# Kernel tuning notes

Hardware: AMD Instinct MI355X
Metric: run time of the kernel (lower is better)

The kernel has to match this reference:

```python
import jax, jax.numpy as jnp
import numpy as np

NUM_HEADS = 16


def setup_inputs() -> dict:
    key = jax.random.key(0)
    ks = jax.random.split(key, 5)
    B, S, E = 4, 2048, 1024
    scale = 1.0 / np.sqrt(E)
    return {
        "query": jax.random.normal(ks[0], (B, S, E), dtype=jnp.float32),
        "w_in": jax.random.normal(ks[1], (3 * E, E), dtype=jnp.float32) * scale,
        "b_in": jax.random.normal(ks[2], (3 * E,), dtype=jnp.float32) * 0.02,
        "w_out": jax.random.normal(ks[3], (E, E), dtype=jnp.float32) * scale,
        "b_out": jax.random.normal(ks[4], (E,), dtype=jnp.float32) * 0.02,
    }


def reference(query, w_in, b_in, w_out, b_out):
    B, S, E = query.shape
    H = NUM_HEADS
    D = E // H
    # fused QKV projection: [B,S,3E]
    qkv = jnp.einsum('bse,fe->bsf', query, w_in) + b_in
    q, k, v = jnp.split(qkv, 3, axis=-1)
    # [B,H,S,D]
    q = q.reshape(B, S, H, D).transpose(0, 2, 1, 3)
    k = k.reshape(B, S, H, D).transpose(0, 2, 1, 3)
    v = v.reshape(B, S, H, D).transpose(0, 2, 1, 3)
    # scaled dot-product attention with causal mask (is_causal=True, dropout=0)
    scores = jnp.einsum('bhqd,bhkd->bhqk', q, k) * (1.0 / np.sqrt(D))
    causal = jnp.tril(jnp.ones((S, S), dtype=bool))
    scores = jnp.where(causal, scores, jnp.finfo(scores.dtype).min)
    probs = jax.nn.softmax(scores, axis=-1)
    attn = jnp.einsum('bhqk,bhkd->bhqd', probs, v)
    attn = attn.transpose(0, 2, 1, 3).reshape(B, S, E)
    return jnp.einsum('bse,fe->bsf', attn, w_out) + b_out
```

## Files before the change

### kernel.cpp

```cpp
#include <hip/hip_runtime.h>

typedef __bf16 bf16;
typedef __bf16 bf16x4 __attribute__((ext_vector_type(4)));
typedef __bf16 bf16x8 __attribute__((ext_vector_type(8)));
typedef float  f32x4  __attribute__((ext_vector_type(4)));
typedef short  short4v __attribute__((ext_vector_type(4)));

#define GLOAD_LDS16(g, l) __builtin_amdgcn_global_load_lds( \
    (const __attribute__((address_space(1))) void*)(g),     \
    (__attribute__((address_space(3))) void*)(l), 16, 0, 0)

__device__ __forceinline__ float exp2_hw(float x) { return __builtin_amdgcn_exp2f(x); }

#if __has_builtin(__builtin_amdgcn_mfma_f32_16x16x16bf16_1k)
__device__ __forceinline__ f32x4 mfma16(bf16x4 a, bf16x4 b, f32x4 c) {
    return __builtin_amdgcn_mfma_f32_16x16x16bf16_1k(
        __builtin_bit_cast(short4v, a), __builtin_bit_cast(short4v, b), c, 0, 0, 0);
}
#elif __has_builtin(__builtin_amdgcn_mfma_f32_16x16x16_bf16)
__device__ __forceinline__ f32x4 mfma16(bf16x4 a, bf16x4 b, f32x4 c) {
    return __builtin_amdgcn_mfma_f32_16x16x16_bf16(a, b, c, 0, 0, 0);
}
#else
__device__ __forceinline__ f32x4 mfma16(bf16x4 a, bf16x4 b, f32x4 c) {
    asm volatile("v_mfma_f32_16x16x16_bf16 %0, %1, %2, %0"
                 : "+v"(c) : "v"(a), "v"(b));
    return c;
}
#endif

__global__ __launch_bounds__(256) void f32_to_bf16(
    const float* __restrict__ in, bf16* __restrict__ out, int n4)
{
    int i = blockIdx.x * blockDim.x + threadIdx.x;
    const int stride = gridDim.x * blockDim.x;
    for (; i < n4; i += stride) {
        const float4 v = *(const float4*)(in + (size_t)i * 4);
        bf16x4 o = { (bf16)v.x, (bf16)v.y, (bf16)v.z, (bf16)v.w };
        *(bf16x4*)(out + (size_t)i * 4) = o;
    }
}

__global__ __launch_bounds__(256) void conv_rest(
    const float* __restrict__ w_in_f, const float* __restrict__ b_in_f,
    const float* __restrict__ w_out_f, const float* __restrict__ b_out_f,
    bf16* __restrict__ w_in, bf16* __restrict__ b_in,
    bf16* __restrict__ w_out, bf16* __restrict__ b_out)
{
    constexpr int N1 = 786432, N2 = N1 + 768, N3 = N2 + 262144, N4 = N3 + 256;
    int i = blockIdx.x * blockDim.x + threadIdx.x;
    const int stride = gridDim.x * blockDim.x;
    for (; i < N4; i += stride) {
        const float* src; bf16* dst; int off;
        if (i < N1)      { src = w_in_f;  dst = w_in;  off = i; }
        else if (i < N2) { src = b_in_f;  dst = b_in;  off = i - N1; }
        else if (i < N3) { src = w_out_f; dst = w_out; off = i - N2; }
        else             { src = b_out_f; dst = b_out; off = i - N3; }
        const float4 v = *(const float4*)(src + (size_t)off * 4);
        bf16x4 o = { (bf16)v.x, (bf16)v.y, (bf16)v.z, (bf16)v.w };
        *(bf16x4*)(dst + (size_t)off * 4) = o;
    }
}

__device__ __forceinline__ void gemm_mainloop_128(
    const bf16* __restrict__ A, const bf16* __restrict__ B, int K,
    int bm, int bn, bf16* As, bf16* Bs, f32x4 (&acc)[4][4])
{
    const int tid  = threadIdx.x;
    const int lane = tid & 63, fr = lane & 15, fq = lane >> 4;
    const int wave = tid >> 6;
    const int wr   = (wave >> 1) * 64, wc = (wave & 1) * 64;
    const int srow = tid >> 3, sj = tid & 7;
    const int sjs  = (sj ^ (srow & 7)) * 8;
    const int xo0  = (fq ^ (fr & 7)) * 8;
    const int xo1  = ((4 + fq) ^ (fr & 7)) * 8;

    const bf16* Ag = A + (size_t)(bm * 128 + srow) * K + sjs;
    const bf16* Bg = B + (size_t)(bn * 128 + srow) * K + sjs;
    bf16* Asw = As + srow * 64 + sj * 8;
    bf16* Bsw = Bs + srow * 64 + sj * 8;

    for (int k0 = 0; k0 < K; k0 += 64) {
        __syncthreads();
#pragma unroll
        for (int it = 0; it < 4; ++it)
            GLOAD_LDS16(Ag + k0 + (size_t)it * 32 * K, Asw + it * 32 * 64);
#pragma unroll
        for (int it = 0; it < 4; ++it)
            GLOAD_LDS16(Bg + k0 + (size_t)it * 32 * K, Bsw + it * 32 * 64);
        asm volatile("s_waitcnt vmcnt(0)" ::: "memory");
        __syncthreads();

#pragma unroll
        for (int ks = 0; ks < 2; ++ks) {
            const int xo = ks ? xo1 : xo0;
            bf16x8 a[4], b[4];
#pragma unroll
            for (int m = 0; m < 4; ++m)
                a[m] = *(const bf16x8*)&As[(wr + m * 16 + fr) * 64 + xo];
#pragma unroll
            for (int n = 0; n < 4; ++n)
                b[n] = *(const bf16x8*)&Bs[(wc + n * 16 + fr) * 64 + xo];
#pragma unroll
            for (int m = 0; m < 4; ++m)
#pragma unroll
                for (int n = 0; n < 4; ++n)
                    acc[m][n] = __builtin_amdgcn_mfma_f32_16x16x32_bf16(a[m], b[n], acc[m][n], 0, 0, 0);
        }
    }
}

__global__ __launch_bounds__(256) void gemm_qkv(
    const bf16* __restrict__ A, const bf16* __restrict__ B,
    const bf16* __restrict__ bias,
    bf16* __restrict__ qb_, bf16* __restrict__ kb_, bf16* __restrict__ vt_)
{
    constexpr int K = 1024, NTN = 24;
    constexpr float QSCALE = 0.18033688011112042f;
    __shared__ bf16 As[128 * 64];
    __shared__ bf16 Bs[128 * 64];
    const int bm = blockIdx.x / NTN, bn = blockIdx.x % NTN;

    f32x4 acc[4][4] = {};
    gemm_mainloop_128(A, B, K, bm, bn, As, Bs, acc);

    const int tid = threadIdx.x, lane = tid & 63;
    const int fr = lane & 15, fq = lane >> 4;
    const int wave = tid >> 6;
    const int wr = (wave >> 1) * 64, wc = (wave & 1) * 64;

    const int colbase = bn * 128 + wc;
    const int part = colbase >> 10;

#pragma unroll
    for (int n = 0; n < 4; ++n) {
        const int col = colbase + n * 16 + fr;
        const float bv = (float)bias[col];
        const int cl = col & 1023, h = cl >> 6, d = cl & 63;
#pragma unroll
        for (int m = 0; m < 4; ++m) {
            const int row0 = bm * 128 + wr + m * 16 + fq * 4;
            const int bb = row0 >> 11, s0 = row0 & 2047;
            const int bh = bb * 16 + h;
            if (part == 0) {
#pragma unroll
                for (int j = 0; j < 4; ++j)
                    qb_[((size_t)bh * 2048 + s0 + j) * 64 + d] = (bf16)((acc[m][n][j] + bv) * QSCALE);
            } else if (part == 1) {
#pragma unroll
                for (int j = 0; j < 4; ++j)
                    kb_[((size_t)bh * 2048 + s0 + j) * 64 + d] = (bf16)(acc[m][n][j] + bv);
            } else {
                bf16x4 o;
#pragma unroll
                for (int j = 0; j < 4; ++j) o[j] = (bf16)(acc[m][n][j] + bv);
                *(bf16x4*)&vt_[((size_t)bh * 64 + d) * 2048 + s0] = o;
            }
        }
    }
}

__global__ __launch_bounds__(256) void gemm_out(
    const bf16* __restrict__ A, const bf16* __restrict__ B,
    const bf16* __restrict__ bias, float* __restrict__ C)
{
    constexpr int K = 1024, N = 1024, NTN = 8;
    __shared__ bf16 As[128 * 64];
    __shared__ bf16 Bs[128 * 64];
    const int bm = blockIdx.x / NTN, bn = blockIdx.x % NTN;

    f32x4 acc[4][4] = {};
    gemm_mainloop_128(A, B, K, bm, bn, As, Bs, acc);

    const int tid = threadIdx.x, lane = tid & 63;
    const int fr = lane & 15, fq = lane >> 4;
    const int wave = tid >> 6;
    const int wr = (wave >> 1) * 64, wc = (wave & 1) * 64;

#pragma unroll
    for (int n = 0; n < 4; ++n) {
        const int col = bn * 128 + wc + n * 16 + fr;
        const float bv = (float)bias[col];
#pragma unroll
        for (int m = 0; m < 4; ++m) {
            const int row0 = bm * 128 + wr + m * 16 + fq * 4;
#pragma unroll
            for (int j = 0; j < 4; ++j)
                C[(size_t)(row0 + j) * N + col] = acc[m][n][j] + bv;
        }
    }
}

__global__ __launch_bounds__(256) void attn4(
    const bf16* __restrict__ qb_, const bf16* __restrict__ kb_,
    const bf16* __restrict__ vt_, bf16* __restrict__ ctx)
{
    constexpr int S = 2048, EO = 1024;
    constexpr float NEG = -3.0e38f;
    __shared__ bf16 Ks[2][64 * 64];
    __shared__ bf16 Vs[2][64 * 64];

    const int idx = blockIdx.x;
    const int orig = (idx & 7) * 256 + (idx >> 3);
    const int bh = orig >> 5;
    const int qb = 31 - (orig & 31);
    const int bb = bh >> 4, h = bh & 15;

    const int tid = threadIdx.x, lane = tid & 63, wave = tid >> 6;
    const int fr = lane & 15, fq = lane >> 4;

    const bf16* kh = kb_ + (size_t)bh * S * 64;
    const bf16* vh = vt_ + (size_t)bh * 64 * S;
    const bf16* qh = qb_ + (size_t)bh * S * 64;

    const int q0 = qb * 64 + wave * 16;

    bf16x8 qf0, qf1;
    {
        const bf16* qr = qh + (size_t)(q0 + fr) * 64;
        qf0 = *(const bf16x8*)(qr + fq * 8);
        qf1 = *(const bf16x8*)(qr + 32 + fq * 8);
    }

    const int xo0 = (fq ^ (fr & 7)) * 8;
    const int xo1 = ((4 + fq) ^ (fr & 7)) * 8;

    int krb[4], vslot[4], vrow[4];
#pragma unroll
    for (int n = 0; n < 4; ++n) {
        krb[n]   = (n * 16 + fr) * 64;
        vslot[n] = ((n * 2 + (fq >> 1)) ^ (fr & 7)) * 8 + (fq & 1) * 4;
        vrow[n]  = (n * 16 + fr) * 64;
    }

    const int r0 = tid >> 3, j0 = tid & 7;
    const int js = (j0 ^ (r0 & 7)) * 8;

#define STAGE(buf, kt)                                                              \
    do {                                                                            \
        GLOAD_LDS16(kh + (size_t)((kt) * 64 + r0) * 64 + js, &Ks[buf][(r0 * 8 + j0) * 8]);        \
        GLOAD_LDS16(kh + (size_t)((kt) * 64 + r0 + 32) * 64 + js, &Ks[buf][((r0 + 32) * 8 + j0) * 8]); \
        GLOAD_LDS16(vh + (size_t)r0 * S + (kt) * 64 + js, &Vs[buf][(r0 * 8 + j0) * 8]);           \
        GLOAD_LDS16(vh + (size_t)(r0 + 32) * S + (kt) * 64 + js, &Vs[buf][((r0 + 32) * 8 + j0) * 8]); \
    } while (0)

    f32x4 acc[4] = {};
    float lrow = 0.0f;

    STAGE(0, 0);
    asm volatile("s_waitcnt vmcnt(0)" ::: "memory");
    __syncthreads();

    int cur = 0;
    for (int kt = 0; kt <= qb; ++kt) {
        if (kt < qb) STAGE(cur ^ 1, kt + 1);

        f32x4 s[4] = {};
        __builtin_amdgcn_s_setprio(1);
#pragma unroll
        for (int n = 0; n < 4; ++n) {
            bf16x8 k0v = *(const bf16x8*)&Ks[cur][krb[n] + xo0];
            bf16x8 k1v = *(const bf16x8*)&Ks[cur][krb[n] + xo1];
            s[n] = __builtin_amdgcn_mfma_f32_16x16x32_bf16(k0v, qf0, s[n], 0, 0, 0);
            s[n] = __builtin_amdgcn_mfma_f32_16x16x32_bf16(k1v, qf1, s[n], 0, 0, 0);
        }
        __builtin_amdgcn_s_setprio(0);

        if (kt == qb) {
            const int qrel = wave * 16 + fr;
#pragma unroll
            for (int n = 0; n < 4; ++n)
#pragma unroll
                for (int j = 0; j < 4; ++j)
                    if (n * 16 + fq * 4 + j > qrel) s[n][j] = NEG;
        }

        bf16x4 pb[4];
        float rs = 0.0f;
#pragma unroll
        for (int n = 0; n < 4; ++n) {
            float p0 = exp2_hw(s[n][0]);
            float p1 = exp2_hw(s[n][1]);
            float p2 = exp2_hw(s[n][2]);
            float p3 = exp2_hw(s[n][3]);
            pb[n][0] = (bf16)p0; pb[n][1] = (bf16)p1;
            pb[n][2] = (bf16)p2; pb[n][3] = (bf16)p3;
            rs += (p0 + p1) + (p2 + p3);
        }
        lrow += rs;

        __builtin_amdgcn_s_setprio(1);
#pragma unroll
        for (int n = 0; n < 4; ++n) {
#pragma unroll
            for (int n2 = 0; n2 < 4; ++n2) {
                bf16x4 vf = *(const bf16x4*)&Vs[cur][vrow[n2] + vslot[n]];
                acc[n2] = mfma16(pb[n], vf, acc[n2]);
            }
        }
        __builtin_amdgcn_s_setprio(0);

        asm volatile("s_waitcnt vmcnt(0)" ::: "memory");
        __syncthreads();
        cur ^= 1;
    }
#undef STAGE

    float l = lrow;
    l += __shfl_xor(l, 16, 64);
    l += __shfl_xor(l, 32, 64);
    float linv[4];
#pragma unroll
    for (int j = 0; j < 4; ++j)
        linv[j] = __builtin_amdgcn_rcpf(__shfl(l, (lane & 48) | (fq * 4 + j), 64));

#pragma unroll
    for (int n2 = 0; n2 < 4; ++n2)
#pragma unroll
        for (int j = 0; j < 4; ++j) {
            int qr_ = q0 + fq * 4 + j;
            ctx[((size_t)bb * S + qr_) * EO + h * 64 + n2 * 16 + fr] = (bf16)(acc[n2][j] * linv[j]);
        }
}

extern "C" void kernel_launch(void* const* d_in, const int* in_sizes, int n_in,
                              void* d_out, int out_size, void* d_ws, size_t ws_size,
                              hipStream_t stream)
{
    constexpr int B = 4, S = 2048, E = 1024;
    constexpr int M = B * S;
    constexpr size_t N_Q  = (size_t)B * S * E;
    constexpr size_t N_WI = (size_t)3 * E * E;
    constexpr size_t N_BI = 3 * E;
    constexpr size_t N_WO = (size_t)E * E;

    const float* query_f = (const float*)d_in[0];
    const float* w_in_f  = (const float*)d_in[1];
    const float* b_in_f  = (const float*)d_in[2];
    const float* w_out_f = (const float*)d_in[3];
    const float* b_out_f = (const float*)d_in[4];
    float* out = (float*)d_out;

    bf16* q_buf = (bf16*)d_ws;
    bf16* k_buf = q_buf + N_Q;
    bf16* vT    = k_buf + N_Q;
    bf16* ctx   = vT + N_Q;
    bf16* query = ctx + N_Q;
    bf16* w_in  = query + N_Q;
    bf16* b_in  = w_in + N_WI;
    bf16* w_out = b_in + N_BI;
    bf16* b_out = w_out + N_WO;

    f32_to_bf16<<<2048, 256, 0, stream>>>(query_f, query, (int)(N_Q / 4));
    conv_rest<<<1024, 256, 0, stream>>>(w_in_f, b_in_f, w_out_f, b_out_f,
                                        w_in, b_in, w_out, b_out);

    gemm_qkv<<<dim3((M / 128) * (3 * E / 128)), 256, 0, stream>>>(
        query, w_in, b_in, q_buf, k_buf, vT);

    attn4<<<dim3(2048), 256, 0, stream>>>(q_buf, k_buf, vT, ctx);

    gemm_out<<<dim3((M / 128) * (E / 128)), 256, 0, stream>>>(
        ctx, w_out, b_out, out);
}
```

Baseline: 188.8 us.

## Enlarge attention query tile to 128 rows with 8 waves and MFMA row sums

The attention kernel now handles 128 query rows per block with 512 threads, so each staged K/V tile in LDS serves twice as many queries and the grid shrinks to 1024 blocks. Each wave skips key sub-tiles that lie entirely above the causal diagonal, and only the diagonal tiles get masked. The softmax row-sum is now computed with an MFMA against a ones vector instead of scalar adds plus cross-lane shuffles. The cost is more threads per block and per-wave imbalance along the diagonal. The sum now also comes from bf16-rounded probabilities.

```diff
diff --git a/kernel.cpp b/kernel.cpp
--- a/kernel.cpp
+++ b/kernel.cpp
@@ -191,7 +191,7 @@
     }
 }
 
-__global__ __launch_bounds__(256) void attn4(
+__global__ __launch_bounds__(512, 8) void attn5(
     const bf16* __restrict__ qb_, const bf16* __restrict__ kb_,
     const bf16* __restrict__ vt_, bf16* __restrict__ ctx)
 {
@@ -201,9 +201,9 @@
     __shared__ bf16 Vs[2][64 * 64];
 
     const int idx = blockIdx.x;
-    const int orig = (idx & 7) * 256 + (idx >> 3);
-    const int bh = orig >> 5;
-    const int qb = 31 - (orig & 31);
+    const int orig = (idx & 7) * 128 + (idx >> 3);
+    const int bh = orig >> 4;
+    const int qb = 15 - (orig & 15);
     const int bb = bh >> 4, h = bh & 15;
 
     const int tid = threadIdx.x, lane = tid & 63, wave = tid >> 6;
@@ -213,7 +213,7 @@
     const bf16* vh = vt_ + (size_t)bh * 64 * S;
     const bf16* qh = qb_ + (size_t)bh * S * 64;
 
-    const int q0 = qb * 64 + wave * 16;
+    const int q0 = qb * 128 + wave * 16;
 
     bf16x8 qf0, qf1;
     {
@@ -236,69 +236,79 @@
     const int r0 = tid >> 3, j0 = tid & 7;
     const int js = (j0 ^ (r0 & 7)) * 8;
 
-#define STAGE(buf, kt)                                                              \
-    do {                                                                            \
-        GLOAD_LDS16(kh + (size_t)((kt) * 64 + r0) * 64 + js, &Ks[buf][(r0 * 8 + j0) * 8]);        \
-        GLOAD_LDS16(kh + (size_t)((kt) * 64 + r0 + 32) * 64 + js, &Ks[buf][((r0 + 32) * 8 + j0) * 8]); \
-        GLOAD_LDS16(vh + (size_t)r0 * S + (kt) * 64 + js, &Vs[buf][(r0 * 8 + j0) * 8]);           \
-        GLOAD_LDS16(vh + (size_t)(r0 + 32) * S + (kt) * 64 + js, &Vs[buf][((r0 + 32) * 8 + j0) * 8]); \
+#define STAGE(buf, kt)                                                        \
+    do {                                                                      \
+        GLOAD_LDS16(kh + (size_t)((kt) * 64 + r0) * 64 + js,                  \
+                    &Ks[buf][(r0 * 8 + j0) * 8]);                             \
+        GLOAD_LDS16(vh + (size_t)r0 * S + (kt) * 64 + js,                     \
+                    &Vs[buf][(r0 * 8 + j0) * 8]);                             \
     } while (0)
 
+    const bf16 one = (bf16)1.0f;
+    const bf16x4 ones = { one, one, one, one };
+
     f32x4 acc[4] = {};
-    float lrow = 0.0f;
+    f32x4 acc1 = {};
+
+    const int ktend = 2 * qb + 1;
 
     STAGE(0, 0);
     asm volatile("s_waitcnt vmcnt(0)" ::: "memory");
     __syncthreads();
 
     int cur = 0;
-    for (int kt = 0; kt <= qb; ++kt) {
-        if (kt < qb) STAGE(cur ^ 1, kt + 1);
-
-        f32x4 s[4] = {};
-        __builtin_amdgcn_s_setprio(1);
-#pragma unroll
-        for (int n = 0; n < 4; ++n) {
-            bf16x8 k0v = *(const bf16x8*)&Ks[cur][krb[n] + xo0];
-            bf16x8 k1v = *(const bf16x8*)&Ks[cur][krb[n] + xo1];
-            s[n] = __builtin_amdgcn_mfma_f32_16x16x32_bf16(k0v, qf0, s[n], 0, 0, 0);
-            s[n] = __builtin_amdgcn_mfma_f32_16x16x32_bf16(k1v, qf1, s[n], 0, 0, 0);
-        }
-        __builtin_amdgcn_s_setprio(0);
-
-        if (kt == qb) {
-            const int qrel = wave * 16 + fr;
-#pragma unroll
-            for (int n = 0; n < 4; ++n)
-#pragma unroll
-                for (int j = 0; j < 4; ++j)
-                    if (n * 16 + fq * 4 + j > qrel) s[n][j] = NEG;
-        }
-
-        bf16x4 pb[4];
-        float rs = 0.0f;
-#pragma unroll
-        for (int n = 0; n < 4; ++n) {
-            float p0 = exp2_hw(s[n][0]);
-            float p1 = exp2_hw(s[n][1]);
-            float p2 = exp2_hw(s[n][2]);
-            float p3 = exp2_hw(s[n][3]);
-            pb[n][0] = (bf16)p0; pb[n][1] = (bf16)p1;
-            pb[n][2] = (bf16)p2; pb[n][3] = (bf16)p3;
-            rs += (p0 + p1) + (p2 + p3);
-        }
-        lrow += rs;
-
-        __builtin_amdgcn_s_setprio(1);
-#pragma unroll
-        for (int n = 0; n < 4; ++n) {
-#pragma unroll
-            for (int n2 = 0; n2 < 4; ++n2) {
-                bf16x4 vf = *(const bf16x4*)&Vs[cur][vrow[n2] + vslot[n]];
-                acc[n2] = mfma16(pb[n], vf, acc[n2]);
-            }
-        }
-        __builtin_amdgcn_s_setprio(0);
+    for (int kt = 0; kt <= ktend; ++kt) {
+        if (kt < ktend) STAGE(cur ^ 1, kt + 1);
+
+        const int nmax = (q0 + 15 - kt * 64) >> 4;
+        if (nmax >= 0) {
+            f32x4 s[4];
+            __builtin_amdgcn_s_setprio(1);
+#pragma unroll
+            for (int n = 0; n < 4; ++n) {
+                if (n > nmax) continue;
+                s[n] = f32x4{};
+                bf16x8 k0v = *(const bf16x8*)&Ks[cur][krb[n] + xo0];
+                bf16x8 k1v = *(const bf16x8*)&Ks[cur][krb[n] + xo1];
+                s[n] = __builtin_amdgcn_mfma_f32_16x16x32_bf16(k0v, qf0, s[n], 0, 0, 0);
+                s[n] = __builtin_amdgcn_mfma_f32_16x16x32_bf16(k1v, qf1, s[n], 0, 0, 0);
+            }
+            __builtin_amdgcn_s_setprio(0);
+
+            if (nmax <= 3) {
+                const int qrel = q0 - kt * 64 + fr;
+#pragma unroll
+                for (int n = 0; n < 4; ++n) {
+                    if (n > nmax) continue;
+#pragma unroll
+                    for (int j = 0; j < 4; ++j)
+                        if (n * 16 + fq * 4 + j > qrel) s[n][j] = NEG;
+                }
+            }
+
+            bf16x4 pb[4];
+#pragma unroll
+            for (int n = 0; n < 4; ++n) {
+                if (n > nmax) continue;
+                pb[n][0] = (bf16)exp2_hw(s[n][0]);
+                pb[n][1] = (bf16)exp2_hw(s[n][1]);
+                pb[n][2] = (bf16)exp2_hw(s[n][2]);
+                pb[n][3] = (bf16)exp2_hw(s[n][3]);
+                acc1 = mfma16(pb[n], ones, acc1);
+            }
+
+            __builtin_amdgcn_s_setprio(1);
+#pragma unroll
+            for (int n = 0; n < 4; ++n) {
+                if (n > nmax) continue;
+#pragma unroll
+                for (int n2 = 0; n2 < 4; ++n2) {
+                    bf16x4 vf = *(const bf16x4*)&Vs[cur][vrow[n2] + vslot[n]];
+                    acc[n2] = mfma16(pb[n], vf, acc[n2]);
+                }
+            }
+            __builtin_amdgcn_s_setprio(0);
+        }
 
         asm volatile("s_waitcnt vmcnt(0)" ::: "memory");
         __syncthreads();
@@ -306,13 +316,9 @@
     }
 #undef STAGE
 
-    float l = lrow;
-    l += __shfl_xor(l, 16, 64);
-    l += __shfl_xor(l, 32, 64);
     float linv[4];
 #pragma unroll
-    for (int j = 0; j < 4; ++j)
-        linv[j] = __builtin_amdgcn_rcpf(__shfl(l, (lane & 48) | (fq * 4 + j), 64));
+    for (int j = 0; j < 4; ++j) linv[j] = __builtin_amdgcn_rcpf(acc1[j]);
 
 #pragma unroll
     for (int n2 = 0; n2 < 4; ++n2)
@@ -358,7 +364,7 @@
     gemm_qkv<<<dim3((M / 128) * (3 * E / 128)), 256, 0, stream>>>(
         query, w_in, b_in, q_buf, k_buf, vT);
 
-    attn4<<<dim3(2048), 256, 0, stream>>>(q_buf, k_buf, vT, ctx);
+    attn5<<<dim3(1024), 512, 0, stream>>>(q_buf, k_buf, vT, ctx);
 
     gemm_out<<<dim3((M / 128) * (E / 128)), 256, 0, stream>>>(
         ctx, w_out, b_out, out);
```

New measurement: 366.6 us. +94.1%, slower.
